# Kernel optimization log

Hardware: AMD Instinct MI355X
Metric: run time of the kernel (lower is better)

Reference implementation:

```python
import jax, jax.numpy as jnp
import numpy as np

EPS = 0.01  # Normalizer eps
N_NODES = 100000
N_EDGES = 1600000


def gcn_conv(x, edge_index, W, b, n_nodes):
    """PyG-style GCNConv: x @ W, symmetric-normalized aggregation with self-loops, + bias."""
    src = jnp.concatenate([edge_index[0], jnp.arange(n_nodes)])  # [E+N]
    dst = jnp.concatenate([edge_index[1], jnp.arange(n_nodes)])  # [E+N]
    h = x @ W  # [N, out]
    ones = jnp.ones_like(dst, dtype=h.dtype)
    deg = jax.ops.segment_sum(ones, dst, num_segments=n_nodes)  # [N]
    dinv = jnp.where(deg > 0, jax.lax.rsqrt(deg), 0.0)
    norm = dinv[src] * dinv[dst]  # [E+N]
    msgs = h[src] * norm[:, None]  # [E+N, out]  (largest intermediate)
    out = jax.ops.segment_sum(msgs, dst, num_segments=n_nodes)  # [N, out]
    return out + b


def setup_inputs() -> dict:
    key = jax.random.key(0)
    k = jax.random.split(key, 6)
    x = jax.random.normal(k[0], (N_NODES, 16), dtype=jnp.float32)
    edge_index = jax.random.randint(k[1], (2, N_EDGES), 0, N_NODES)
    W1 = jax.random.normal(k[2], (16, 64), dtype=jnp.float32) * 0.25
    b1 = jax.random.normal(k[3], (64,), dtype=jnp.float32) * 0.1
    W3 = jax.random.normal(k[4], (64, 32), dtype=jnp.float32) * 0.125
    b3 = jax.random.normal(k[5], (32,), dtype=jnp.float32) * 0.1
    return {"x": x, "edge_index": edge_index, "W1": W1, "b1": b1, "W3": W3, "b3": b3}


def reference(x, edge_index, W1, b1, W3, b3):
    n = x.shape[0]
    h = jax.nn.relu(gcn_conv(x, edge_index, W1, b1, n))
    h = jax.nn.relu(gcn_conv(h, edge_index, W3, b3, n))
    # Normalizer: sequential Welford observe over all nodes then normalize with
    # FINAL stats == population mean / clamped population variance.
    mean = h.mean(axis=0)  # [32]
    var = jnp.maximum(((h - mean) ** 2).mean(axis=0), EPS)  # [32]
    return (h - mean) * jax.lax.rsqrt(var)
```

## Files before the change

### kernel.cpp

```cpp
#include <hip/hip_runtime.h>
#include <hip/hip_fp16.h>

#define EPS 0.01f
#define SCAN_BS 512
#define NCHUNKS 256
#define BUCKET_SHIFT 8
#define BUCKET_SZ (1 << BUCKET_SHIFT)
#define STAGE_CAP 6144


__global__ __launch_bounds__(SCAN_BS) void k_scan_block(const int* __restrict__ in,
                                                        int* __restrict__ out,
                                                        int* __restrict__ bsum, int n) {
    __shared__ int sd[SCAN_BS];
    int t = threadIdx.x;
    int gid = blockIdx.x * SCAN_BS + t;
    int v = (gid < n) ? in[gid] : 0;
    sd[t] = v;
    __syncthreads();
    for (int off = 1; off < SCAN_BS; off <<= 1) {
        int x = (t >= off) ? sd[t - off] : 0;
        __syncthreads();
        sd[t] += x;
        __syncthreads();
    }
    if (gid < n) out[gid] = sd[t] - v;
    if (t == SCAN_BS - 1) bsum[blockIdx.x] = sd[t];
}

__global__ __launch_bounds__(SCAN_BS) void k_scan_tops(int* __restrict__ bsum, int nb) {
    __shared__ int sd[SCAN_BS];
    int t = threadIdx.x;
    int v = (t < nb) ? bsum[t] : 0;
    sd[t] = v;
    __syncthreads();
    for (int off = 1; off < SCAN_BS; off <<= 1) {
        int x = (t >= off) ? sd[t - off] : 0;
        __syncthreads();
        sd[t] += x;
        __syncthreads();
    }
    if (t < nb) bsum[t] = sd[t] - v;
}

__global__ __launch_bounds__(SCAN_BS) void k_scan_add(int* __restrict__ out,
                                                      const int* __restrict__ bsum, int n) {
    int gid = blockIdx.x * SCAN_BS + threadIdx.x;
    if (gid < n) out[gid] += bsum[blockIdx.x];
}


__global__ __launch_bounds__(256) void kA_bucket_hist(const int* __restrict__ dst,
                                                      int* __restrict__ bh, int e,
                                                      int nbuck, int ce) {
    extern __shared__ int hist[];
    int b = blockIdx.x, t = threadIdx.x;
    for (int i = t; i < nbuck; i += 256) hist[i] = 0;
    __syncthreads();
    int lo = b * ce, hi = min(lo + ce, e);
    int len = hi - lo;
    if (len > 0) {
        int len4 = len & ~3;
        for (int i = t * 4; i < len4; i += 1024) {
            int4 d4 = *(const int4*)(dst + lo + i);
            atomicAdd(&hist[d4.x >> BUCKET_SHIFT], 1);
            atomicAdd(&hist[d4.y >> BUCKET_SHIFT], 1);
            atomicAdd(&hist[d4.z >> BUCKET_SHIFT], 1);
            atomicAdd(&hist[d4.w >> BUCKET_SHIFT], 1);
        }
        for (int i = len4 + t; i < len; i += 256)
            atomicAdd(&hist[dst[lo + i] >> BUCKET_SHIFT], 1);
    }
    __syncthreads();
    for (int i = t; i < nbuck; i += 256) bh[i * NCHUNKS + b] = hist[i];
}

__global__ __launch_bounds__(256) void kC_bucket_scatter(const int* __restrict__ src,
                                                         const int* __restrict__ dst,
                                                         const int* __restrict__ bhs,
                                                         unsigned int* __restrict__ eb, int e,
                                                         int nbuck, int ce) {
    extern __shared__ int cur[];
    int b = blockIdx.x, t = threadIdx.x;
    for (int i = t; i < nbuck; i += 256) cur[i] = bhs[i * NCHUNKS + b];
    __syncthreads();
    int lo = b * ce, hi = min(lo + ce, e);
    int len = hi - lo;
    if (len > 0) {
        int len4 = len & ~3;
        for (int i = t * 4; i < len4; i += 1024) {
            int4 s4 = *(const int4*)(src + lo + i);
            int4 d4 = *(const int4*)(dst + lo + i);
            int p0 = atomicAdd(&cur[d4.x >> BUCKET_SHIFT], 1);
            eb[p0] = ((unsigned int)(d4.x & (BUCKET_SZ - 1)) << 23) | (unsigned int)s4.x;
            int p1 = atomicAdd(&cur[d4.y >> BUCKET_SHIFT], 1);
            eb[p1] = ((unsigned int)(d4.y & (BUCKET_SZ - 1)) << 23) | (unsigned int)s4.y;
            int p2 = atomicAdd(&cur[d4.z >> BUCKET_SHIFT], 1);
            eb[p2] = ((unsigned int)(d4.z & (BUCKET_SZ - 1)) << 23) | (unsigned int)s4.z;
            int p3 = atomicAdd(&cur[d4.w >> BUCKET_SHIFT], 1);
            eb[p3] = ((unsigned int)(d4.w & (BUCKET_SZ - 1)) << 23) | (unsigned int)s4.w;
        }
        for (int i = len4 + t; i < len; i += 256) {
            int s = src[lo + i], d = dst[lo + i];
            int pos = atomicAdd(&cur[d >> BUCKET_SHIFT], 1);
            eb[pos] = ((unsigned int)(d & (BUCKET_SZ - 1)) << 23) | (unsigned int)s;
        }
    }
}

__global__ __launch_bounds__(256) void kDeg_fill_prescale(const unsigned int* __restrict__ eb,
                                                          const int* __restrict__ bhs,
                                                          const float* __restrict__ x,
                                                          int* __restrict__ degi,
                                                          float* __restrict__ dinv,
                                                          int* __restrict__ rowstart,
                                                          int* __restrict__ csr_src,
                                                          __half* __restrict__ xs,
                                                          float* __restrict__ partial,
                                                          int n, int nbuck, int e) {
    __shared__ unsigned int ebs[STAGE_CAP];
    __shared__ int hist[BUCKET_SZ];
    __shared__ int ps[BUCKET_SZ];
    __shared__ float dv[BUCKET_SZ];
    int k = blockIdx.x, t = threadIdx.x;
    if (k == 0 && t < 64) partial[t] = 0.f;
    hist[t] = 0;
    __syncthreads();
    int lo = bhs[k * NCHUNKS];
    int hi = (k + 1 < nbuck) ? bhs[(k + 1) * NCHUNKS] : e;
    int cnt = hi - lo;
    bool fits = (cnt <= STAGE_CAP);
    for (int i = t; i < cnt; i += 256) {
        unsigned int p = eb[lo + i];
        if (fits) ebs[i] = p;
        atomicAdd(&hist[p >> 23], 1);
    }
    __syncthreads();
    int a0 = hist[t];
    ps[t] = a0;
    __syncthreads();
    for (int off = 1; off < 256; off <<= 1) {
        int v = (t >= off) ? ps[t - off] : 0;
        __syncthreads();
        ps[t] += v;
        __syncthreads();
    }
    int excl = ps[t] - a0;
    int node0 = k << BUCKET_SHIFT;
    int rs0 = lo + excl;
    float d0 = rsqrtf((float)a0 + 1.0f);
    dv[t] = d0;
    {
        int nd = node0 + t;
        if (nd < n) {
            degi[nd] = a0;
            dinv[nd] = d0;
            rowstart[nd] = rs0;
        }
    }
    __syncthreads();
    hist[t] = rs0;
    {
        const float2* xf2 = (const float2*)x;
        __half2* xs2 = (__half2*)xs;
        for (int i = t; i < BUCKET_SZ * 8; i += 256) {
            int rl = i >> 3;
            int node = node0 + rl;
            if (node < n) {
                float2 vv = xf2[(size_t)node * 8 + (i & 7)];
                float d = dv[rl];
                xs2[(size_t)node * 8 + (i & 7)] = __floats2half2_rn(vv.x * d, vv.y * d);
            }
        }
    }
    __syncthreads();
    for (int i = t; i < cnt; i += 256) {
        unsigned int p = fits ? ebs[i] : eb[lo + i];
        int dl = (int)(p >> 23);
        int s = (int)(p & 0x7fffffu);
        int pos = atomicAdd(&hist[dl], 1);
        csr_src[pos] = s;
    }
}


__global__ __launch_bounds__(256) void k_l1_fused(const int* __restrict__ rowstart,
                                                  const int* __restrict__ degi,
                                                  const int* __restrict__ csr_src,
                                                  const float* __restrict__ dinv,
                                                  const __half* __restrict__ xs,
                                                  const float* __restrict__ W1,
                                                  const float* __restrict__ b1,
                                                  const float* __restrict__ W3,
                                                  __half* __restrict__ h2s, int n) {
    __shared__ float w1[16 * 64];
    __shared__ float w3[64 * 32];
    __shared__ float bs[64];
    __shared__ __align__(16) float a[16 * 16];
    __shared__ float z[16 * 64];
    int t = threadIdx.x;
    for (int i = t; i < 16 * 64; i += 256) w1[i] = W1[i];
    for (int i = t; i < 64 * 32; i += 256) w3[i] = W3[i];
    if (t < 64) bs[t] = b1[t];

    int row0 = blockIdx.x * 16;
    int wv = t >> 6;
    int lane = t & 63;
    int c2 = lane & 7;
    int slot = lane >> 3;
    const __half2* xs2 = (const __half2*)xs;

    int nb = row0 + wv * 4;
    int node = nb;
    int rs_c = 0, dg_c = 0;
    if (node < n) { rs_c = rowstart[node]; dg_c = degi[node]; }
    for (int nid = 0; nid < 4; ++nid) {
        int node_nxt = nb + nid + 1;
        int rs_n = 0, dg_n = 0;
        if (nid < 3 && node_nxt < n) { rs_n = rowstart[node_nxt]; dg_n = degi[node_nxt]; }
        if (node < n) {
            float dn = dinv[node];
            float2 self = __half22float2(xs2[(size_t)node * 8 + c2]);
            const int* sp = csr_src + rs_c;
            int deg = dg_c;
            int L = (deg + 7) >> 3;
            int base = slot * L;
            int end = min(base + L, deg);
            float ax = 0.f, ay = 0.f, bx = 0.f, by = 0.f;
            int k = base;
            for (; k + 2 <= end; k += 2) {
                int s0 = sp[k], s1 = sp[k + 1];
                float2 v0 = __half22float2(xs2[(size_t)s0 * 8 + c2]);
                float2 v1 = __half22float2(xs2[(size_t)s1 * 8 + c2]);
                ax += v0.x; ay += v0.y;
                bx += v1.x; by += v1.y;
            }
            if (k < end) {
                int s0 = sp[k];
                float2 v0 = __half22float2(xs2[(size_t)s0 * 8 + c2]);
                ax += v0.x; ay += v0.y;
            }
            float sx = ax + bx, sy = ay + by;
            sx += __shfl_xor(sx, 8);  sy += __shfl_xor(sy, 8);
            sx += __shfl_xor(sx, 16); sy += __shfl_xor(sy, 16);
            sx += __shfl_xor(sx, 32); sy += __shfl_xor(sy, 32);
            if (slot == 0) {
                int r = wv * 4 + nid;
                ((float2*)(a + r * 16))[c2] = make_float2(dn * (sx + self.x), dn * (sy + self.y));
            }
        }
        node = node_nxt; rs_c = rs_n; dg_c = dg_n;
    }
    __syncthreads();

    for (int i = t; i < 1024; i += 256) {
        int r = i >> 6, c = i & 63;
        float acc = bs[c];
#pragma unroll
        for (int k = 0; k < 16; ++k) acc += a[r * 16 + k] * w1[k * 64 + c];
        z[i] = acc > 0.f ? acc : 0.f;
    }
    __syncthreads();
    for (int i = t; i < 512; i += 256) {
        int r = i >> 5, c = i & 31;
        float acc = 0.f;
#pragma unroll
        for (int k = 0; k < 64; ++k) acc += z[r * 64 + k] * w3[k * 32 + c];
        int row = row0 + r;
        if (row < n) h2s[(size_t)row * 32 + c] = __float2half(acc * dinv[row]);
    }
}


__global__ __launch_bounds__(256) void k_gather32_stats(const int* __restrict__ rowstart,
                                                        const int* __restrict__ degi,
                                                        const int* __restrict__ csr_src,
                                                        const float* __restrict__ dinv,
                                                        const __half* __restrict__ h2s,
                                                        const float* __restrict__ b3,
                                                        float* __restrict__ out,
                                                        float* __restrict__ partial, int n) {
    int t = threadIdx.x;
    int lane = t & 63;
    int c2 = lane & 15;
    int slot = lane >> 4;
    const __half2* h2 = (const __half2*)h2s;
    float2 bias = ((const float2*)b3)[c2];
    float s_x = 0.f, s_y = 0.f, q_x = 0.f, q_y = 0.f;

    int node = blockIdx.x * 32 + (t >> 6);
    int rs_c = 0, dg_c = 0;
    if (node < n) { rs_c = rowstart[node]; dg_c = degi[node]; }
    for (int it = 0; it < 8; ++it) {
        int node_nxt = node + 4;
        int rs_n = 0, dg_n = 0;
        if (it < 7 && node_nxt < n) { rs_n = rowstart[node_nxt]; dg_n = degi[node_nxt]; }
        if (node < n) {
            float dn = dinv[node];
            float2 self = __half22float2(h2[(size_t)node * 16 + c2]);
            const int* sp = csr_src + rs_c;
            int deg = dg_c;
            int L = (deg + 3) >> 2;
            int base = slot * L;
            int end = min(base + L, deg);
            float ax = 0.f, ay = 0.f, bx = 0.f, by = 0.f;
            float cx = 0.f, cy = 0.f, dx = 0.f, dy = 0.f;
            int k = base;
            for (; k + 4 <= end; k += 4) {
                int s0 = sp[k], s1 = sp[k + 1], s2 = sp[k + 2], s3 = sp[k + 3];
                float2 v0 = __half22float2(h2[(size_t)s0 * 16 + c2]);
                float2 v1 = __half22float2(h2[(size_t)s1 * 16 + c2]);
                float2 v2 = __half22float2(h2[(size_t)s2 * 16 + c2]);
                float2 v3 = __half22float2(h2[(size_t)s3 * 16 + c2]);
                ax += v0.x; ay += v0.y;
                bx += v1.x; by += v1.y;
                cx += v2.x; cy += v2.y;
                dx += v3.x; dy += v3.y;
            }
            for (; k < end; ++k) {
                int s0 = sp[k];
                float2 v0 = __half22float2(h2[(size_t)s0 * 16 + c2]);
                ax += v0.x; ay += v0.y;
            }
            float sx = (ax + bx) + (cx + dx);
            float sy = (ay + by) + (cy + dy);
            sx += __shfl_xor(sx, 16); sy += __shfl_xor(sy, 16);
            sx += __shfl_xor(sx, 32); sy += __shfl_xor(sy, 32);
            if (slot == 0) {
                float vx = dn * (sx + self.x) + bias.x;
                float vy = dn * (sy + self.y) + bias.y;
                vx = vx > 0.f ? vx : 0.f;
                vy = vy > 0.f ? vy : 0.f;
                ((float2*)(out + (size_t)node * 32))[c2] = make_float2(vx, vy);
                s_x += vx; s_y += vy;
                q_x += vx * vx; q_y += vy * vy;
            }
        }
        node = node_nxt; rs_c = rs_n; dg_c = dg_n;
    }
    __shared__ float ls[128], lq[128];
    int wv = t >> 6;
    if ((t & 63) < 16) {
        ls[wv * 32 + 2 * c2] = s_x;
        ls[wv * 32 + 2 * c2 + 1] = s_y;
        lq[wv * 32 + 2 * c2] = q_x;
        lq[wv * 32 + 2 * c2 + 1] = q_y;
    }
    __syncthreads();
    if (t < 32) {
        float a = 0.f, b = 0.f;
#pragma unroll
        for (int w = 0; w < 4; ++w) {
            a += ls[w * 32 + t];
            b += lq[w * 32 + t];
        }
        atomicAdd(&partial[t], a);
        atomicAdd(&partial[32 + t], b);
    }
}


__global__ void k_norm(float* __restrict__ h, const float* __restrict__ partial, int n) {
    __shared__ __align__(16) float mv[64];
    int t = threadIdx.x;
    if (t < 32) {
        float invn = 1.0f / (float)n;
        float mean = partial[t] * invn;
        float var = partial[32 + t] * invn - mean * mean;
        var = var > EPS ? var : EPS;
        mv[t] = mean;
        mv[32 + t] = rsqrtf(var);
    }
    __syncthreads();
    int idx = blockIdx.x * blockDim.x + threadIdx.x;
    if (idx < n * 8) {
        int c4 = idx & 7;
        float4 v = ((float4*)h)[idx];
        float4 m = ((const float4*)mv)[c4];
        float4 iv = ((const float4*)(mv + 32))[c4];
        v.x = (v.x - m.x) * iv.x;
        v.y = (v.y - m.y) * iv.y;
        v.z = (v.z - m.z) * iv.z;
        v.w = (v.w - m.w) * iv.w;
        ((float4*)h)[idx] = v;
    }
}

extern "C" void kernel_launch(void* const* d_in, const int* in_sizes, int n_in,
                              void* d_out, int out_size, void* d_ws, size_t ws_size,
                              hipStream_t stream) {
    const float* x  = (const float*)d_in[0];
    const int* ei   = (const int*)d_in[1];
    const float* W1 = (const float*)d_in[2];
    const float* b1 = (const float*)d_in[3];
    const float* W3 = (const float*)d_in[4];
    const float* b3 = (const float*)d_in[5];

    const int N = in_sizes[0] / 16;
    const int E = in_sizes[1] / 2;
    const int* src = ei;
    const int* dst = ei + E;

    const int NBUCK = (N + BUCKET_SZ - 1) >> BUCKET_SHIFT;
    int CE = (E + NCHUNKS - 1) / NCHUNKS;
    CE = (CE + 3) & ~3;
    const int BH_TOTAL = NBUCK * NCHUNKS;

    char* ws = (char*)d_ws;
    int*   degi     = (int*)ws;          ws += (size_t)N * 4;
    float* dinv     = (float*)ws;        ws += (size_t)N * 4;
    int*   rowstart = (int*)ws;          ws += (size_t)N * 4;
    int*   bsum2    = (int*)ws;          ws += (size_t)SCAN_BS * 4;
    int*   bh       = (int*)ws;          ws += (size_t)BH_TOTAL * 4;
    int*   bhs      = (int*)ws;          ws += (size_t)BH_TOTAL * 4;
    unsigned int* eb = (unsigned int*)ws; ws += (size_t)E * 4;
    int*   csr_src  = (int*)ws;          ws += (size_t)E * 4;
    __half* xs      = (__half*)ws;       ws += (size_t)N * 16 * 2;
    __half* h2s     = (__half*)ws;       ws += (size_t)N * 32 * 2;
    float* partial  = (float*)ws;        ws += 64 * 4;

    float* out = (float*)d_out;

    const int NB2 = (BH_TOTAL + SCAN_BS - 1) / SCAN_BS;

    kA_bucket_hist<<<NCHUNKS, 256, NBUCK * 4, stream>>>(dst, bh, E, NBUCK, CE);
    k_scan_block<<<NB2, SCAN_BS, 0, stream>>>(bh, bhs, bsum2, BH_TOTAL);
    k_scan_tops<<<1, SCAN_BS, 0, stream>>>(bsum2, NB2);
    k_scan_add<<<NB2, SCAN_BS, 0, stream>>>(bhs, bsum2, BH_TOTAL);
    kC_bucket_scatter<<<NCHUNKS, 256, NBUCK * 4, stream>>>(src, dst, bhs, eb, E, NBUCK, CE);

    kDeg_fill_prescale<<<NBUCK, 256, 0, stream>>>(eb, bhs, x, degi, dinv, rowstart,
                                                  csr_src, xs, partial, N, NBUCK, E);

    k_l1_fused<<<(N + 15) / 16, 256, 0, stream>>>(rowstart, degi, csr_src, dinv, xs,
                                                  W1, b1, W3, h2s, N);

    k_gather32_stats<<<(N + 31) / 32, 256, 0, stream>>>(rowstart, degi, csr_src, dinv, h2s,
                                                        b3, out, partial, N);

    k_norm<<<(N * 8 + 255) / 256, 256, 0, stream>>>(out, partial, N);
}
```

Measured before the change: 167.6 us.

## Fuse bucket histogram and scatter using fixed-capacity buckets with global atomic cursors

```diff
diff --git a/kernel.cpp b/kernel.cpp
--- a/kernel.cpp
+++ b/kernel.cpp
@@ -2,87 +2,31 @@
 #include <hip/hip_fp16.h>
 
 #define EPS 0.01f
-#define SCAN_BS 512
-#define NCHUNKS 256
+#define NCHUNKS2 512
 #define BUCKET_SHIFT 8
 #define BUCKET_SZ (1 << BUCKET_SHIFT)
+#define CAP 6144
 #define STAGE_CAP 6144
 
 
-__global__ __launch_bounds__(SCAN_BS) void k_scan_block(const int* __restrict__ in,
-                                                        int* __restrict__ out,
-                                                        int* __restrict__ bsum, int n) {
-    __shared__ int sd[SCAN_BS];
-    int t = threadIdx.x;
-    int gid = blockIdx.x * SCAN_BS + t;
-    int v = (gid < n) ? in[gid] : 0;
-    sd[t] = v;
-    __syncthreads();
-    for (int off = 1; off < SCAN_BS; off <<= 1) {
-        int x = (t >= off) ? sd[t - off] : 0;
-        __syncthreads();
-        sd[t] += x;
-        __syncthreads();
-    }
-    if (gid < n) out[gid] = sd[t] - v;
-    if (t == SCAN_BS - 1) bsum[blockIdx.x] = sd[t];
-}
-
-__global__ __launch_bounds__(SCAN_BS) void k_scan_tops(int* __restrict__ bsum, int nb) {
-    __shared__ int sd[SCAN_BS];
-    int t = threadIdx.x;
-    int v = (t < nb) ? bsum[t] : 0;
-    sd[t] = v;
-    __syncthreads();
-    for (int off = 1; off < SCAN_BS; off <<= 1) {
-        int x = (t >= off) ? sd[t - off] : 0;
-        __syncthreads();
-        sd[t] += x;
-        __syncthreads();
-    }
-    if (t < nb) bsum[t] = sd[t] - v;
-}
-
-__global__ __launch_bounds__(SCAN_BS) void k_scan_add(int* __restrict__ out,
-                                                      const int* __restrict__ bsum, int n) {
-    int gid = blockIdx.x * SCAN_BS + threadIdx.x;
-    if (gid < n) out[gid] += bsum[blockIdx.x];
-}
-
-
-__global__ __launch_bounds__(256) void kA_bucket_hist(const int* __restrict__ dst,
-                                                      int* __restrict__ bh, int e,
-                                                      int nbuck, int ce) {
-    extern __shared__ int hist[];
+__global__ void k_zero_cursors(int* __restrict__ gcur, int nbuck) {
+    int i = blockIdx.x * blockDim.x + threadIdx.x;
+    if (i < nbuck) gcur[i] = 0;
+}
+
+
+__global__ __launch_bounds__(256) void kAC_fused(const int* __restrict__ src,
+                                                 const int* __restrict__ dst,
+                                                 int* __restrict__ gcur,
+                                                 unsigned int* __restrict__ eb,
+                                                 int e, int nbuck, int ce) {
+    extern __shared__ int lds[];
+    int* ss = lds;
+    int* dd = ss + ce;
+    int* hist = dd + ce;
+    int* cur = hist + nbuck;
     int b = blockIdx.x, t = threadIdx.x;
     for (int i = t; i < nbuck; i += 256) hist[i] = 0;
-    __syncthreads();
-    int lo = b * ce, hi = min(lo + ce, e);
-    int len = hi - lo;
-    if (len > 0) {
-        int len4 = len & ~3;
-        for (int i = t * 4; i < len4; i += 1024) {
-            int4 d4 = *(const int4*)(dst + lo + i);
-            atomicAdd(&hist[d4.x >> BUCKET_SHIFT], 1);
-            atomicAdd(&hist[d4.y >> BUCKET_SHIFT], 1);
-            atomicAdd(&hist[d4.z >> BUCKET_SHIFT], 1);
-            atomicAdd(&hist[d4.w >> BUCKET_SHIFT], 1);
-        }
-        for (int i = len4 + t; i < len; i += 256)
-            atomicAdd(&hist[dst[lo + i] >> BUCKET_SHIFT], 1);
-    }
-    __syncthreads();
-    for (int i = t; i < nbuck; i += 256) bh[i * NCHUNKS + b] = hist[i];
-}
-
-__global__ __launch_bounds__(256) void kC_bucket_scatter(const int* __restrict__ src,
-                                                         const int* __restrict__ dst,
-                                                         const int* __restrict__ bhs,
-                                                         unsigned int* __restrict__ eb, int e,
-                                                         int nbuck, int ce) {
-    extern __shared__ int cur[];
-    int b = blockIdx.x, t = threadIdx.x;
-    for (int i = t; i < nbuck; i += 256) cur[i] = bhs[i * NCHUNKS + b];
     __syncthreads();
     int lo = b * ce, hi = min(lo + ce, e);
     int len = hi - lo;
@@ -91,25 +35,35 @@
         for (int i = t * 4; i < len4; i += 1024) {
             int4 s4 = *(const int4*)(src + lo + i);
             int4 d4 = *(const int4*)(dst + lo + i);
-            int p0 = atomicAdd(&cur[d4.x >> BUCKET_SHIFT], 1);
-            eb[p0] = ((unsigned int)(d4.x & (BUCKET_SZ - 1)) << 23) | (unsigned int)s4.x;
-            int p1 = atomicAdd(&cur[d4.y >> BUCKET_SHIFT], 1);
-            eb[p1] = ((unsigned int)(d4.y & (BUCKET_SZ - 1)) << 23) | (unsigned int)s4.y;
-            int p2 = atomicAdd(&cur[d4.z >> BUCKET_SHIFT], 1);
-            eb[p2] = ((unsigned int)(d4.z & (BUCKET_SZ - 1)) << 23) | (unsigned int)s4.z;
-            int p3 = atomicAdd(&cur[d4.w >> BUCKET_SHIFT], 1);
-            eb[p3] = ((unsigned int)(d4.w & (BUCKET_SZ - 1)) << 23) | (unsigned int)s4.w;
+            *(int4*)(ss + i) = s4;
+            *(int4*)(dd + i) = d4;
+            atomicAdd(&hist[d4.x >> BUCKET_SHIFT], 1);
+            atomicAdd(&hist[d4.y >> BUCKET_SHIFT], 1);
+            atomicAdd(&hist[d4.z >> BUCKET_SHIFT], 1);
+            atomicAdd(&hist[d4.w >> BUCKET_SHIFT], 1);
         }
         for (int i = len4 + t; i < len; i += 256) {
             int s = src[lo + i], d = dst[lo + i];
-            int pos = atomicAdd(&cur[d >> BUCKET_SHIFT], 1);
-            eb[pos] = ((unsigned int)(d & (BUCKET_SZ - 1)) << 23) | (unsigned int)s;
-        }
+            ss[i] = s; dd[i] = d;
+            atomicAdd(&hist[d >> BUCKET_SHIFT], 1);
+        }
+    }
+    __syncthreads();
+    for (int i = t; i < nbuck; i += 256) {
+        int h = hist[i];
+        int base = h ? atomicAdd(&gcur[i], h) : 0;
+        cur[i] = i * CAP + base;
+    }
+    __syncthreads();
+    for (int i = t; i < len; i += 256) {
+        int d = dd[i];
+        int pos = atomicAdd(&cur[d >> BUCKET_SHIFT], 1);
+        eb[pos] = ((unsigned int)(d & (BUCKET_SZ - 1)) << 23) | (unsigned int)ss[i];
     }
 }
 
 __global__ __launch_bounds__(256) void kDeg_fill_prescale(const unsigned int* __restrict__ eb,
-                                                          const int* __restrict__ bhs,
+                                                          const int* __restrict__ gcur,
                                                           const float* __restrict__ x,
                                                           int* __restrict__ degi,
                                                           float* __restrict__ dinv,
@@ -117,8 +71,8 @@
                                                           int* __restrict__ csr_src,
                                                           __half* __restrict__ xs,
                                                           float* __restrict__ partial,
-                                                          int n, int nbuck, int e) {
-    __shared__ unsigned int ebs[STAGE_CAP];
+                                                          int n, int nbuck) {
+    __shared__ __align__(16) unsigned int ebs[STAGE_CAP];
     __shared__ int hist[BUCKET_SZ];
     __shared__ int ps[BUCKET_SZ];
     __shared__ float dv[BUCKET_SZ];
@@ -126,13 +80,20 @@
     if (k == 0 && t < 64) partial[t] = 0.f;
     hist[t] = 0;
     __syncthreads();
-    int lo = bhs[k * NCHUNKS];
-    int hi = (k + 1 < nbuck) ? bhs[(k + 1) * NCHUNKS] : e;
-    int cnt = hi - lo;
-    bool fits = (cnt <= STAGE_CAP);
-    for (int i = t; i < cnt; i += 256) {
+    int lo = k * CAP;
+    int cnt = min(gcur[k], CAP);
+    int cnt4 = cnt & ~3;
+    for (int i = t * 4; i < cnt4; i += 1024) {
+        uint4 p4 = *(const uint4*)(eb + lo + i);
+        *(uint4*)(ebs + i) = p4;
+        atomicAdd(&hist[p4.x >> 23], 1);
+        atomicAdd(&hist[p4.y >> 23], 1);
+        atomicAdd(&hist[p4.z >> 23], 1);
+        atomicAdd(&hist[p4.w >> 23], 1);
+    }
+    for (int i = cnt4 + t; i < cnt; i += 256) {
         unsigned int p = eb[lo + i];
-        if (fits) ebs[i] = p;
+        ebs[i] = p;
         atomicAdd(&hist[p >> 23], 1);
     }
     __syncthreads();
@@ -175,7 +136,7 @@
     }
     __syncthreads();
     for (int i = t; i < cnt; i += 256) {
-        unsigned int p = fits ? ebs[i] : eb[lo + i];
+        unsigned int p = ebs[i];
         int dl = (int)(p >> 23);
         int s = (int)(p & 0x7fffffu);
         int pos = atomicAdd(&hist[dl], 1);
@@ -402,35 +363,28 @@
     const int* dst = ei + E;
 
     const int NBUCK = (N + BUCKET_SZ - 1) >> BUCKET_SHIFT;
-    int CE = (E + NCHUNKS - 1) / NCHUNKS;
+    int CE = (E + NCHUNKS2 - 1) / NCHUNKS2;
     CE = (CE + 3) & ~3;
-    const int BH_TOTAL = NBUCK * NCHUNKS;
 
     char* ws = (char*)d_ws;
     int*   degi     = (int*)ws;          ws += (size_t)N * 4;
     float* dinv     = (float*)ws;        ws += (size_t)N * 4;
     int*   rowstart = (int*)ws;          ws += (size_t)N * 4;
-    int*   bsum2    = (int*)ws;          ws += (size_t)SCAN_BS * 4;
-    int*   bh       = (int*)ws;          ws += (size_t)BH_TOTAL * 4;
-    int*   bhs      = (int*)ws;          ws += (size_t)BH_TOTAL * 4;
-    unsigned int* eb = (unsigned int*)ws; ws += (size_t)E * 4;
-    int*   csr_src  = (int*)ws;          ws += (size_t)E * 4;
+    int*   gcur     = (int*)ws;          ws += (size_t)NBUCK * 4;
+    unsigned int* eb = (unsigned int*)ws; ws += (size_t)NBUCK * CAP * 4;
+    int*   csr_src  = (int*)ws;          ws += (size_t)NBUCK * CAP * 4;
     __half* xs      = (__half*)ws;       ws += (size_t)N * 16 * 2;
     __half* h2s     = (__half*)ws;       ws += (size_t)N * 32 * 2;
     float* partial  = (float*)ws;        ws += 64 * 4;
 
     float* out = (float*)d_out;
 
-    const int NB2 = (BH_TOTAL + SCAN_BS - 1) / SCAN_BS;
-
-    kA_bucket_hist<<<NCHUNKS, 256, NBUCK * 4, stream>>>(dst, bh, E, NBUCK, CE);
-    k_scan_block<<<NB2, SCAN_BS, 0, stream>>>(bh, bhs, bsum2, BH_TOTAL);
-    k_scan_tops<<<1, SCAN_BS, 0, stream>>>(bsum2, NB2);
-    k_scan_add<<<NB2, SCAN_BS, 0, stream>>>(bhs, bsum2, BH_TOTAL);
-    kC_bucket_scatter<<<NCHUNKS, 256, NBUCK * 4, stream>>>(src, dst, bhs, eb, E, NBUCK, CE);
-
-    kDeg_fill_prescale<<<NBUCK, 256, 0, stream>>>(eb, bhs, x, degi, dinv, rowstart,
-                                                  csr_src, xs, partial, N, NBUCK, E);
+    k_zero_cursors<<<(NBUCK + 255) / 256, 256, 0, stream>>>(gcur, NBUCK);
+    const size_t kac_lds = (size_t)(2 * CE + 2 * NBUCK) * 4;
+    kAC_fused<<<NCHUNKS2, 256, kac_lds, stream>>>(src, dst, gcur, eb, E, NBUCK, CE);
+
+    kDeg_fill_prescale<<<NBUCK, 256, 0, stream>>>(eb, gcur, x, degi, dinv, rowstart,
+                                                  csr_src, xs, partial, N, NBUCK);
 
     k_l1_fused<<<(N + 15) / 16, 256, 0, stream>>>(rowstart, degi, csr_src, dinv, xs,
                                                   W1, b1, W3, h2s, N);
```

Result: slower. 220.9 us (+31.9%).
